# Kernel optimization log

Measured on AMD Instinct MI355X. Metric: run time of the kernel, lower is better.

The kernel has to match this reference:

```python
import jax, jax.numpy as jnp
import numpy as np
from jax import lax

B = 256
C1 = 256          # conv1 channels
NUM_CAPS = 32     # primary capsule types
CAP_DIM = 8       # primary capsule dim
NUM_PRIMARY = NUM_CAPS * 6 * 6  # 1152
NUM_OUT = 10
OUT_DIM = 16
NUM_ROUTING = 3


def squash(v):
    # v: (..., d)
    sq = jnp.sum(v * v, axis=-1, keepdims=True)
    scale = sq / (1.0 + sq)
    return scale * v / jnp.sqrt(sq + 1e-8)


def setup_inputs() -> dict:
    key = jax.random.key(0)
    k = jax.random.split(key, 6)
    x = jax.random.normal(k[0], (B, 1, 28, 28), dtype=jnp.float32)
    # kaiming fan_out init for convs
    conv1_w = jax.random.normal(k[1], (C1, 1, 9, 9), dtype=jnp.float32) * np.sqrt(2.0 / (C1 * 81))
    conv1_b = jnp.zeros((C1,), dtype=jnp.float32)
    pc_out = NUM_CAPS * CAP_DIM  # 256
    pc_w = jax.random.normal(k[2], (pc_out, C1, 9, 9), dtype=jnp.float32) * np.sqrt(2.0 / (pc_out * 81))
    pc_b = jnp.zeros((pc_out,), dtype=jnp.float32)
    W_digit = jax.random.normal(k[3], (NUM_PRIMARY, CAP_DIM, NUM_OUT, OUT_DIM), dtype=jnp.float32) * 0.01
    return {"x": x, "conv1_w": conv1_w, "conv1_b": conv1_b,
            "pc_w": pc_w, "pc_b": pc_b, "W_digit": W_digit}


def _conv(x, w, b, stride):
    y = lax.conv_general_dilated(x, w, (stride, stride), 'VALID',
                                 dimension_numbers=('NCHW', 'OIHW', 'NCHW'))
    return y + b[None, :, None, None]


def reference(x, conv1_w, conv1_b, pc_w, pc_b, W_digit):
    # conv1 + ReLU: (B,1,28,28) -> (B,256,20,20)
    h = jax.nn.relu(_conv(x, conv1_w, conv1_b, 1))
    # primary caps conv: -> (B, 256, 6, 6)
    p = _conv(h, pc_w, pc_b, 2)
    bsz, _, oh, ow = p.shape
    # (B, num_caps, cap_dim, H, W) -> (B, num_caps, H, W, cap_dim) -> (B, N, d)
    p = p.reshape(bsz, NUM_CAPS, CAP_DIM, oh, ow)
    p = jnp.transpose(p, (0, 1, 3, 4, 2)).reshape(bsz, NUM_CAPS * oh * ow, CAP_DIM)
    u = squash(p)  # (B, 1152, 8)
    # dynamic routing
    u_hat = jnp.einsum('bid,idjo->bijo', u, W_digit)  # (B, 1152, 10, 16)
    b_logits = jnp.zeros((bsz, NUM_PRIMARY, NUM_OUT, 1), dtype=u_hat.dtype)
    v = None
    for it in range(NUM_ROUTING):
        c = jax.nn.softmax(b_logits, axis=2)
        s = jnp.sum(c * u_hat, axis=1)          # (B, 10, 16)
        v = squash(s)
        if it < NUM_ROUTING - 1:
            agreement = jnp.sum(u_hat * v[:, None, :, :], axis=-1, keepdims=True)
            b_logits = b_logits + agreement
    return v
```

## Files before the change

kernel.cpp:

```cpp
#include <hip/hip_runtime.h>
#include <hip/hip_bf16.h>

#define NI 1152

typedef __attribute__((ext_vector_type(8))) _Float16 f16x8;
typedef __attribute__((ext_vector_type(4))) float f32x4;
typedef __attribute__((ext_vector_type(8))) unsigned short u16x8;
typedef __attribute__((ext_vector_type(4))) unsigned short u16x4;

static const size_t UHAT_OFF = 0;
static const size_t W5_OFF   = 0;
static const size_t H3_OFF   = 10747904UL;
static const size_t WT1_OFF  = 63176704UL;
static const size_t PP_OFF   = 63259648UL;
static const size_t U_OFF    = 94371840UL;
static const size_t SP_OFF   = 103809024UL;
static const size_t L_OFF    = 127401984UL;
static const size_t V_OFF    = 139198464UL;

__device__ __forceinline__ unsigned short f2bf(float x) {
    unsigned u = __builtin_bit_cast(unsigned, x);
    u += 0x7fffu + ((u >> 16) & 1u);
    return (unsigned short)(u >> 16);
}
__device__ __forceinline__ float bf2f(unsigned short h) {
    return __builtin_bit_cast(float, (unsigned)h << 16);
}
__device__ __forceinline__ void atomAddF(float* p, float v) {
    __hip_atomic_fetch_add(p, v, __ATOMIC_RELAXED, __HIP_MEMORY_SCOPE_AGENT);
}

#define GLD16(gsrc, ldst)                                                      \
    __builtin_amdgcn_global_load_lds(                                          \
        (__attribute__((address_space(1))) const void*)(gsrc),                 \
        (__attribute__((address_space(3))) void*)(ldst), 16, 0, 0)

__global__ __launch_bounds__(256) void k_prep_w(const float* __restrict__ pcw,
                                                _Float16* __restrict__ w5) {
    __shared__ float sl[5184];
    int oc  = blockIdx.x;
    int ic0 = blockIdx.y * 64;
    const float* src = pcw + (size_t)oc * 20736 + (size_t)ic0 * 81;
    for (int j = threadIdx.x; j < 5184; j += 256) sl[j] = src[j];
    __syncthreads();
    int nt = oc >> 7, row = oc & 127;
    for (int t = threadIdx.x; t < 5184; t += 256) {
        int tap = t >> 6, i = t & 63;
        int ic = ic0 + i;
        int ks = ic >> 5, p = (ic >> 3) & 3, icl = ic & 7;
        w5[((size_t)(((tap * 8 + ks) * 2 + nt) * 4 + p) * 128 + row) * 8 + icl] =
            (_Float16)sl[i * 81 + tap];
    }
}

__global__ void k_transpose_w1(const float* __restrict__ w, float* __restrict__ wT) {
    int t = blockIdx.x, oc = threadIdx.x;
    wT[t * 256 + oc] = w[oc * 81 + t];
}

__global__ __launch_bounds__(256) void k_conv1(const float* __restrict__ x,
                                               const float* __restrict__ wT1,
                                               const float* __restrict__ bias,
                                               _Float16* __restrict__ h3) {
    __shared__ _Float16 hs[2][20][256];
    int b  = blockIdx.y;
    int rp = blockIdx.x;
    int oc = threadIdx.x;
    int oy0 = rp * 2;
    const float* xb = x + (size_t)b * 784;
    float bv = bias[oc];
    float acc0[20], acc1[20];
#pragma unroll
    for (int i = 0; i < 20; ++i) { acc0[i] = bv; acc1[i] = bv; }
    for (int ky = 0; ky < 9; ++ky) {
        const float* r0 = xb + (oy0 + ky) * 28;
        const float* r1 = r0 + 28;
        float x0[28], x1[28];
#pragma unroll
        for (int c = 0; c < 28; ++c) { x0[c] = r0[c]; x1[c] = r1[c]; }
#pragma unroll
        for (int kx = 0; kx < 9; ++kx) {
            float w = wT1[(ky * 9 + kx) * 256 + oc];
#pragma unroll
            for (int px = 0; px < 20; ++px) {
                acc0[px] += x0[px + kx] * w;
                acc1[px] += x1[px + kx] * w;
            }
        }
    }
#pragma unroll
    for (int px = 0; px < 20; ++px) {
        hs[0][px][oc] = (_Float16)fmaxf(acc0[px], 0.f);
        hs[1][px][oc] = (_Float16)fmaxf(acc1[px], 0.f);
    }
    __syncthreads();
    for (int cid = threadIdx.x; cid < 1280; cid += 256) {
        int kp = cid & 31;
        int pos = cid >> 5;
        int ry = pos / 20, px2 = pos % 20;
        int ks = kp >> 2, p = kp & 3;
        f16x8 val = *(const f16x8*)&hs[ry][px2][ks * 32 + p * 8];
        _Float16* dst = h3 + ((size_t)((ks * 400 + (oy0 + ry) * 20 + px2) * 4 + p) * 256 + b) * 8;
        *(f16x8*)dst = val;
    }
}

__global__ __launch_bounds__(256, 4) void k_conv2_mfma(
    const _Float16* __restrict__ h3, const _Float16* __restrict__ w5,
    float* __restrict__ pp) {
    __shared__ _Float16 As[8192], Bs[8192];
    const int mt = blockIdx.x, nt = blockIdx.y, ks = blockIdx.z;
    const int pos = mt >> 1, bhalf = mt & 1;
    const int py = pos / 6, px = pos % 6;
    const int l = threadIdx.x & 63;
    const int w = __builtin_amdgcn_readfirstlane((int)(threadIdx.x >> 6));
    const int wm = w >> 1, wn = w & 1;

    f32x4 acc[4][4];
    const f32x4 z = {0.f, 0.f, 0.f, 0.f};
#pragma unroll
    for (int mi = 0; mi < 4; ++mi)
#pragma unroll
        for (int ni = 0; ni < 4; ++ni) acc[mi][ni] = z;

    const int ch = (l >> 4) * 1024;
    const int am = (wm * 64 + (l & 15)) * 8;
    const int bn = (wn * 64 + (l & 15)) * 8;
    const int lds_off = w * 1024 + l * 8;

    for (int it = 0; it < 41; ++it) {
        const int t0 = 2 * it, t1 = t0 + 1;
        const int tA1 = (t1 > 80) ? 80 : t1;
#pragma unroll
        for (int tl = 0; tl < 2; ++tl) {
            const int tap  = tl ? t1 : t0;
            const int tapA = tl ? tA1 : t0;
            const int y = 2 * py + tapA / 9, xx = 2 * px + tapA % 9;
            const _Float16* asrc = h3 + ((size_t)(ks * 400 + y * 20 + xx) * 4 + w) * 2048 +
                                   bhalf * 1024 + l * 8;
            const _Float16* bsrc = w5 + ((size_t)((tap * 8 + ks) * 2 + nt)) * 4096 + lds_off;
            GLD16(asrc,       As + tl * 4096 + lds_off);
            GLD16(asrc + 512, As + tl * 4096 + lds_off + 512);
            GLD16(bsrc,       Bs + tl * 4096 + lds_off);
            GLD16(bsrc + 512, Bs + tl * 4096 + lds_off + 512);
        }
        __syncthreads();
#pragma unroll
        for (int s = 0; s < 2; ++s) {
            const int pb = s * 4096 + ch;
            f16x8 a[4], b[4];
#pragma unroll
            for (int i = 0; i < 4; ++i) {
                a[i] = *(const f16x8*)(As + pb + am + i * 128);
                b[i] = *(const f16x8*)(Bs + pb + bn + i * 128);
            }
#pragma unroll
            for (int mi = 0; mi < 4; ++mi)
#pragma unroll
                for (int ni = 0; ni < 4; ++ni)
                    acc[mi][ni] = __builtin_amdgcn_mfma_f32_16x16x32_f16(a[mi], b[ni], acc[mi][ni], 0, 0, 0);
        }
        __syncthreads();
    }
    const int row0 = (l >> 4) * 4;
    const int ncol = l & 15;
#pragma unroll
    for (int mi = 0; mi < 4; ++mi)
#pragma unroll
        for (int ni = 0; ni < 4; ++ni) {
            int n = nt * 128 + wn * 64 + ni * 16 + ncol;
#pragma unroll
            for (int reg = 0; reg < 4; ++reg) {
                int m = pos * 256 + bhalf * 128 + wm * 64 + mi * 16 + row0 + reg;
                atomAddF(&pp[(size_t)m * 256 + n], acc[mi][ni][reg]);
            }
        }
}

__global__ __launch_bounds__(256) void k_sum_squash2(const float* __restrict__ pp,
                                                     const float* __restrict__ bias,
                                                     float* __restrict__ u) {
    int m = blockIdx.x * 8 + (threadIdx.x >> 5);
    int cap = threadIdx.x & 31;
    const float* p0 = pp + (size_t)m * 256 + cap * 8;
    float s[8], sq = 0.f;
#pragma unroll
    for (int d = 0; d < 8; ++d) {
        float a = p0[d] + bias[cap * 8 + d];
        sq += a * a; s[d] = a;
    }
    float scale = sq / ((1.0f + sq) * sqrtf(sq + 1e-8f));
    int pos = m >> 8, b = m & 255;
    int i = cap * 36 + pos;
    float* up = u + ((size_t)i * 256 + b) * 8;
    ((float4*)up)[0] = make_float4(scale * s[0], scale * s[1], scale * s[2], scale * s[3]);
    ((float4*)up)[1] = make_float4(scale * s[4], scale * s[5], scale * s[6], scale * s[7]);
}

__global__ __launch_bounds__(256) void k_build_uhat(const float* __restrict__ u,
                                                    const float* __restrict__ W,
                                                    unsigned short* __restrict__ UH) {
    __shared__ float Ws[1280];
    int i = blockIdx.x;
    for (int t = threadIdx.x; t < 1280; t += 256) Ws[t] = W[(size_t)i * 1280 + t];
    __syncthreads();
    int b = threadIdx.x;
    const float* uptr = u + ((size_t)i * 256 + b) * 8;
    float u8[8];
    ((float4*)u8)[0] = ((const float4*)uptr)[0];
    ((float4*)u8)[1] = ((const float4*)uptr)[1];
#pragma unroll
    for (int j = 0; j < 10; ++j) {
        float o16[16];
#pragma unroll
        for (int o = 0; o < 16; ++o) o16[o] = 0.f;
#pragma unroll
        for (int d = 0; d < 8; ++d) {
            const float* wp = Ws + d * 160 + j * 16;
#pragma unroll
            for (int o = 0; o < 16; ++o) o16[o] += u8[d] * wp[o];
        }
        u16x8 h0, h1;
#pragma unroll
        for (int o = 0; o < 8; ++o) { h0[o] = f2bf(o16[o]); h1[o] = f2bf(o16[8 + o]); }
        unsigned short* dst = UH + ((size_t)(i * 10 + j) * 256 + b) * 16;
        *(u16x8*)dst = h0;
        *(u16x8*)(dst + 8) = h1;
    }
}

__global__ __launch_bounds__(256) void k_route_s0(const unsigned short* __restrict__ UH,
                                                  float* __restrict__ SP) {
    int it = blockIdx.x, bt = blockIdx.y;
    int b0 = bt * 64, i0 = it * 8;
    int b_l = threadIdx.x & 63;
    int og = __builtin_amdgcn_readfirstlane((int)(threadIdx.x >> 6));
    float acc[10][4];
#pragma unroll
    for (int j = 0; j < 10; ++j)
#pragma unroll
        for (int o = 0; o < 4; ++o) acc[j][o] = 0.f;
    for (int li = 0; li < 8; ++li) {
        const unsigned short* up = UH + ((size_t)(i0 + li) * 10 * 256 + b0 + b_l) * 16 + og * 4;
#pragma unroll
        for (int j = 0; j < 10; ++j) {
            u16x4 t = *(const u16x4*)(up + j * 4096);
#pragma unroll
            for (int o = 0; o < 4; ++o) acc[j][o] += bf2f(t[o]);
        }
    }
    float* sp = SP + ((size_t)it * 256 + b0 + b_l) * 160 + og * 4;
#pragma unroll
    for (int j = 0; j < 10; ++j)
        *(float4*)(sp + j * 16) = make_float4(0.1f * acc[j][0], 0.1f * acc[j][1],
                                              0.1f * acc[j][2], 0.1f * acc[j][3]);
}

__global__ __launch_bounds__(256) void k_route_s(const float* __restrict__ L,
                                                 const unsigned short* __restrict__ UH,
                                                 float* __restrict__ SP) {
    __shared__ float LG[64][81];
    int it = blockIdx.x, bt = blockIdx.y;
    int b0 = bt * 64, i0 = it * 8;
    int b_l = threadIdx.x & 63;
    int og = __builtin_amdgcn_readfirstlane((int)(threadIdx.x >> 6));
    int b_r = threadIdx.x >> 2, part = threadIdx.x & 3;
    {
        const float4* lsrc = (const float4*)(L + (size_t)(b0 + b_r) * 11520 + i0 * 10 + part * 20);
#pragma unroll
        for (int q = 0; q < 5; ++q) {
            float4 t = lsrc[q]; int c = part * 20 + q * 4;
            LG[b_r][c] = t.x; LG[b_r][c + 1] = t.y; LG[b_r][c + 2] = t.z; LG[b_r][c + 3] = t.w;
        }
    }
    __syncthreads();
    float acc[10][4];
#pragma unroll
    for (int j = 0; j < 10; ++j)
#pragma unroll
        for (int o = 0; o < 4; ++o) acc[j][o] = 0.f;
    for (int li = 0; li < 8; ++li) {
        float lg[10];
#pragma unroll
        for (int j = 0; j < 10; ++j) lg[j] = LG[b_l][li * 10 + j];
        float m = lg[0];
#pragma unroll
        for (int j = 1; j < 10; ++j) m = fmaxf(m, lg[j]);
        float e[10], ssum = 0.f;
#pragma unroll
        for (int j = 0; j < 10; ++j) { e[j] = __expf(lg[j] - m); ssum += e[j]; }
        float inv = 1.0f / ssum;
        const unsigned short* up = UH + ((size_t)(i0 + li) * 10 * 256 + b0 + b_l) * 16 + og * 4;
#pragma unroll
        for (int j = 0; j < 10; ++j) {
            float cj = e[j] * inv;
            u16x4 t = *(const u16x4*)(up + j * 4096);
#pragma unroll
            for (int o = 0; o < 4; ++o) acc[j][o] += cj * bf2f(t[o]);
        }
    }
    float* sp = SP + ((size_t)it * 256 + b0 + b_l) * 160 + og * 4;
#pragma unroll
    for (int j = 0; j < 10; ++j)
        *(float4*)(sp + j * 16) = make_float4(acc[j][0], acc[j][1], acc[j][2], acc[j][3]);
}

__global__ __launch_bounds__(256) void k_route_v(const float* __restrict__ SP,
                                                 float* __restrict__ vout) {
    int n = blockIdx.x * 256 + threadIdx.x;
    float ssum = 0.f;
    for (int t = 0; t < 144; ++t) ssum += SP[(size_t)t * 40960 + n];
    float sq = ssum * ssum;
    float tot = sq;
#pragma unroll
    for (int mask = 1; mask < 16; mask <<= 1) tot += __shfl_xor(tot, mask, 64);
    float scale = tot / ((1.0f + tot) * sqrtf(tot + 1e-8f));
    vout[n] = scale * ssum;
}

__global__ __launch_bounds__(256) void k_route_agree(float* __restrict__ L,
                                                     const unsigned short* __restrict__ UH,
                                                     const float* __restrict__ V,
                                                     int add) {
    __shared__ float VL[64][165];
    __shared__ float LG[64][81];
    int it = blockIdx.x, bt = blockIdx.y;
    int b0 = bt * 64, i0 = it * 8;
    int b_l = threadIdx.x & 63;
    int ig = __builtin_amdgcn_readfirstlane((int)(threadIdx.x >> 6));
    int b_r = threadIdx.x >> 2, part = threadIdx.x & 3;
    {
        const float4* vsrc = (const float4*)(V + (size_t)(b0 + b_r) * 160 + part * 40);
#pragma unroll
        for (int q = 0; q < 10; ++q) {
            float4 vv = vsrc[q]; int c = part * 40 + q * 4;
            VL[b_r][c] = vv.x; VL[b_r][c + 1] = vv.y; VL[b_r][c + 2] = vv.z; VL[b_r][c + 3] = vv.w;
        }
        if (add) {
            const float4* lsrc = (const float4*)(L + (size_t)(b0 + b_r) * 11520 + i0 * 10 + part * 20);
#pragma unroll
            for (int q = 0; q < 5; ++q) {
                float4 t = lsrc[q]; int c = part * 20 + q * 4;
                LG[b_r][c] = t.x; LG[b_r][c + 1] = t.y; LG[b_r][c + 2] = t.z; LG[b_r][c + 3] = t.w;
            }
        }
    }
    __syncthreads();
#pragma unroll
    for (int ii = 0; ii < 2; ++ii) {
        int il = ig * 2 + ii;
        int i = i0 + il;
        const unsigned short* up = UH + ((size_t)i * 10 * 256 + b0 + b_l) * 16;
#pragma unroll
        for (int j = 0; j < 10; ++j) {
            u16x8 ua = *(const u16x8*)(up + j * 4096);
            u16x8 ub = *(const u16x8*)(up + j * 4096 + 8);
            float a = 0.f;
#pragma unroll
            for (int o = 0; o < 8; ++o) a += bf2f(ua[o]) * VL[b_l][j * 16 + o];
#pragma unroll
            for (int o = 0; o < 8; ++o) a += bf2f(ub[o]) * VL[b_l][j * 16 + 8 + o];
            float base = add ? LG[b_l][il * 10 + j] : 0.f;
            LG[b_l][il * 10 + j] = base + a;
        }
    }
    __syncthreads();
    {
        float4* ldst = (float4*)(L + (size_t)(b0 + b_r) * 11520 + i0 * 10 + part * 20);
#pragma unroll
        for (int q = 0; q < 5; ++q) {
            int c = part * 20 + q * 4;
            ldst[q] = make_float4(LG[b_r][c], LG[b_r][c + 1], LG[b_r][c + 2], LG[b_r][c + 3]);
        }
    }
}

extern "C" void kernel_launch(void* const* d_in, const int* in_sizes, int n_in,
                              void* d_out, int out_size, void* d_ws, size_t ws_size,
                              hipStream_t stream) {
    (void)in_sizes; (void)n_in; (void)out_size; (void)ws_size;
    const float* x   = (const float*)d_in[0];
    const float* c1w = (const float*)d_in[1];
    const float* c1b = (const float*)d_in[2];
    const float* pcw = (const float*)d_in[3];
    const float* pcb = (const float*)d_in[4];
    const float* Wd  = (const float*)d_in[5];
    float* out = (float*)d_out;
    char* wsb  = (char*)d_ws;

    unsigned short* uh = (unsigned short*)(wsb + UHAT_OFF);
    _Float16* w5 = (_Float16*)(wsb + W5_OFF);
    _Float16* h3 = (_Float16*)(wsb + H3_OFF);
    float* wT1 = (float*)(wsb + WT1_OFF);
    float* pp  = (float*)(wsb + PP_OFF);
    float* u   = (float*)(wsb + U_OFF);
    float* sp  = (float*)(wsb + SP_OFF);
    float* lg  = (float*)(wsb + L_OFF);
    float* v   = (float*)(wsb + V_OFF);

    hipMemsetAsync(pp, 0, (size_t)9216 * 256 * sizeof(float), stream);
    hipMemsetAsync(w5 + (size_t)81 * 65536, 0, (size_t)65536 * sizeof(_Float16), stream);

    k_prep_w<<<dim3(256, 4), 256, 0, stream>>>(pcw, w5);
    k_transpose_w1<<<81, 256, 0, stream>>>(c1w, wT1);
    k_conv1<<<dim3(10, 256), 256, 0, stream>>>(x, wT1, c1b, h3);
    k_conv2_mfma<<<dim3(72, 2, 8), 256, 0, stream>>>(h3, w5, pp);
    k_sum_squash2<<<1152, 256, 0, stream>>>(pp, pcb, u);
    k_build_uhat<<<1152, 256, 0, stream>>>(u, Wd, uh);

    k_route_s0<<<dim3(144, 4), 256, 0, stream>>>(uh, sp);
    k_route_v<<<160, 256, 0, stream>>>(sp, v);
    k_route_agree<<<dim3(144, 4), 256, 0, stream>>>(lg, uh, v, 0);
    k_route_s<<<dim3(144, 4), 256, 0, stream>>>(lg, uh, sp);
    k_route_v<<<160, 256, 0, stream>>>(sp, v);
    k_route_agree<<<dim3(144, 4), 256, 0, stream>>>(lg, uh, v, 1);
    k_route_s<<<dim3(144, 4), 256, 0, stream>>>(lg, uh, sp);
    k_route_v<<<160, 256, 0, stream>>>(sp, out);
}
```

Baseline: 474.7 us.

## Load conv2 MFMA operands directly to registers and fuse routing agree with softmax-sum

The primary-capsule conv now reads A and B fragments straight from global memory into registers with a three-stage software pipeline. This replaces the LDS staging and barriers, and the weights are re-laid out so each lane's fragment is contiguous. The routing agreement and the next iteration's softmax-weighted sum are fused into one kernel that reuses the logits held in LDS, which removes a kernel launch and a global round trip of the logits per iteration. The trade-off is heavier register pressure (occupancy hint lowered to 2) and less global-load coalescing and reuse for the A operand.

```diff
diff --git a/kernel.cpp b/kernel.cpp
--- a/kernel.cpp
+++ b/kernel.cpp
@@ -9,7 +9,7 @@
 typedef __attribute__((ext_vector_type(4))) unsigned short u16x4;
 
 static const size_t UHAT_OFF = 0;
-static const size_t W5_OFF   = 0;
+static const size_t W6_OFF   = 0;
 static const size_t H3_OFF   = 10747904UL;
 static const size_t WT1_OFF  = 63176704UL;
 static const size_t PP_OFF   = 63259648UL;
@@ -30,25 +30,21 @@
     __hip_atomic_fetch_add(p, v, __ATOMIC_RELAXED, __HIP_MEMORY_SCOPE_AGENT);
 }
 
-#define GLD16(gsrc, ldst)                                                      \
-    __builtin_amdgcn_global_load_lds(                                          \
-        (__attribute__((address_space(1))) const void*)(gsrc),                 \
-        (__attribute__((address_space(3))) void*)(ldst), 16, 0, 0)
-
 __global__ __launch_bounds__(256) void k_prep_w(const float* __restrict__ pcw,
-                                                _Float16* __restrict__ w5) {
+                                                _Float16* __restrict__ w6) {
     __shared__ float sl[5184];
     int oc  = blockIdx.x;
     int ic0 = blockIdx.y * 64;
     const float* src = pcw + (size_t)oc * 20736 + (size_t)ic0 * 81;
     for (int j = threadIdx.x; j < 5184; j += 256) sl[j] = src[j];
     __syncthreads();
-    int nt = oc >> 7, row = oc & 127;
+    int og = oc >> 4, fr = oc & 15;
     for (int t = threadIdx.x; t < 5184; t += 256) {
         int tap = t >> 6, i = t & 63;
         int ic = ic0 + i;
-        int ks = ic >> 5, p = (ic >> 3) & 3, icl = ic & 7;
-        w5[((size_t)(((tap * 8 + ks) * 2 + nt) * 4 + p) * 128 + row) * 8 + icl] =
+        int ks = ic >> 5, kch = (ic >> 3) & 3, icl = ic & 7;
+        int lane = kch * 16 + fr;
+        w6[(((size_t)(tap * 8 + ks) * 16 + og) * 64 + lane) * 8 + icl] =
             (_Float16)sl[i * 81 + tap];
     }
 }
@@ -105,17 +101,22 @@
     }
 }
 
-__global__ __launch_bounds__(256, 4) void k_conv2_mfma(
-    const _Float16* __restrict__ h3, const _Float16* __restrict__ w5,
+__global__ __launch_bounds__(256, 2) void k_conv2_direct(
+    const _Float16* __restrict__ h3, const _Float16* __restrict__ w6,
     float* __restrict__ pp) {
-    __shared__ _Float16 As[8192], Bs[8192];
     const int mt = blockIdx.x, nt = blockIdx.y, ks = blockIdx.z;
     const int pos = mt >> 1, bhalf = mt & 1;
     const int py = pos / 6, px = pos % 6;
     const int l = threadIdx.x & 63;
-    const int w = __builtin_amdgcn_readfirstlane((int)(threadIdx.x >> 6));
+    const int w = threadIdx.x >> 6;
     const int wm = w >> 1, wn = w & 1;
-
+    const int p = l >> 4, fr = l & 15;
+
+    const _Float16* abase = h3 + (size_t)ks * 3276800 + p * 2048 +
+                            (bhalf * 128 + wm * 64 + fr) * 8;
+    const _Float16* bbase = w6 + (nt * 8 + wn * 4) * 512 + l * 8;
+
+    f16x8 a[3][4], b[3][4];
     f32x4 acc[4][4];
     const f32x4 z = {0.f, 0.f, 0.f, 0.f};
 #pragma unroll
@@ -123,45 +124,44 @@
 #pragma unroll
         for (int ni = 0; ni < 4; ++ni) acc[mi][ni] = z;
 
-    const int ch = (l >> 4) * 1024;
-    const int am = (wm * 64 + (l & 15)) * 8;
-    const int bn = (wn * 64 + (l & 15)) * 8;
-    const int lds_off = w * 1024 + l * 8;
-
-    for (int it = 0; it < 41; ++it) {
-        const int t0 = 2 * it, t1 = t0 + 1;
-        const int tA1 = (t1 > 80) ? 80 : t1;
-#pragma unroll
-        for (int tl = 0; tl < 2; ++tl) {
-            const int tap  = tl ? t1 : t0;
-            const int tapA = tl ? tA1 : t0;
-            const int y = 2 * py + tapA / 9, xx = 2 * px + tapA % 9;
-            const _Float16* asrc = h3 + ((size_t)(ks * 400 + y * 20 + xx) * 4 + w) * 2048 +
-                                   bhalf * 1024 + l * 8;
-            const _Float16* bsrc = w5 + ((size_t)((tap * 8 + ks) * 2 + nt)) * 4096 + lds_off;
-            GLD16(asrc,       As + tl * 4096 + lds_off);
-            GLD16(asrc + 512, As + tl * 4096 + lds_off + 512);
-            GLD16(bsrc,       Bs + tl * 4096 + lds_off);
-            GLD16(bsrc + 512, Bs + tl * 4096 + lds_off + 512);
-        }
-        __syncthreads();
-#pragma unroll
-        for (int s = 0; s < 2; ++s) {
-            const int pb = s * 4096 + ch;
-            f16x8 a[4], b[4];
-#pragma unroll
-            for (int i = 0; i < 4; ++i) {
-                a[i] = *(const f16x8*)(As + pb + am + i * 128);
-                b[i] = *(const f16x8*)(Bs + pb + bn + i * 128);
-            }
-#pragma unroll
-            for (int mi = 0; mi < 4; ++mi)
-#pragma unroll
-                for (int ni = 0; ni < 4; ++ni)
-                    acc[mi][ni] = __builtin_amdgcn_mfma_f32_16x16x32_f16(a[mi], b[ni], acc[mi][ni], 0, 0, 0);
-        }
-        __syncthreads();
-    }
+#define LOADAB(buf, tap)                                                       \
+    do {                                                                       \
+        const int _t = (tap);                                                  \
+        const int _y = _t / 9, _x = _t - _y * 9;                               \
+        const _Float16* _ab = abase + ((2 * py + _y) * 20 + (2 * px + _x)) * 8192; \
+        a[buf][0] = *(const f16x8*)(_ab);                                      \
+        a[buf][1] = *(const f16x8*)(_ab + 128);                                \
+        a[buf][2] = *(const f16x8*)(_ab + 256);                                \
+        a[buf][3] = *(const f16x8*)(_ab + 384);                                \
+        const _Float16* _bb = bbase + (size_t)(_t * 8 + ks) * 8192;            \
+        b[buf][0] = *(const f16x8*)(_bb);                                      \
+        b[buf][1] = *(const f16x8*)(_bb + 512);                                \
+        b[buf][2] = *(const f16x8*)(_bb + 1024);                               \
+        b[buf][3] = *(const f16x8*)(_bb + 1536);                               \
+    } while (0)
+
+#define MFMA_ALL(buf)                                                          \
+    do {                                                                       \
+        _Pragma("unroll") for (int mi = 0; mi < 4; ++mi)                       \
+            _Pragma("unroll") for (int ni = 0; ni < 4; ++ni)                   \
+                acc[mi][ni] = __builtin_amdgcn_mfma_f32_16x16x32_f16(          \
+                    a[buf][mi], b[buf][ni], acc[mi][ni], 0, 0, 0);             \
+    } while (0)
+
+    LOADAB(0, 0);
+    LOADAB(1, 1);
+    for (int k = 0; k < 27; ++k) {
+        const int t0 = 3 * k;
+        LOADAB(2, t0 + 2);
+        MFMA_ALL(0);
+        if (t0 + 3 < 81) LOADAB(0, t0 + 3);
+        MFMA_ALL(1);
+        if (t0 + 4 < 81) LOADAB(1, t0 + 4);
+        MFMA_ALL(2);
+    }
+#undef LOADAB
+#undef MFMA_ALL
+
     const int row0 = (l >> 4) * 4;
     const int ncol = l & 15;
 #pragma unroll
@@ -256,72 +256,11 @@
                                               0.1f * acc[j][2], 0.1f * acc[j][3]);
 }
 
-__global__ __launch_bounds__(256) void k_route_s(const float* __restrict__ L,
-                                                 const unsigned short* __restrict__ UH,
-                                                 float* __restrict__ SP) {
-    __shared__ float LG[64][81];
-    int it = blockIdx.x, bt = blockIdx.y;
-    int b0 = bt * 64, i0 = it * 8;
-    int b_l = threadIdx.x & 63;
-    int og = __builtin_amdgcn_readfirstlane((int)(threadIdx.x >> 6));
-    int b_r = threadIdx.x >> 2, part = threadIdx.x & 3;
-    {
-        const float4* lsrc = (const float4*)(L + (size_t)(b0 + b_r) * 11520 + i0 * 10 + part * 20);
-#pragma unroll
-        for (int q = 0; q < 5; ++q) {
-            float4 t = lsrc[q]; int c = part * 20 + q * 4;
-            LG[b_r][c] = t.x; LG[b_r][c + 1] = t.y; LG[b_r][c + 2] = t.z; LG[b_r][c + 3] = t.w;
-        }
-    }
-    __syncthreads();
-    float acc[10][4];
-#pragma unroll
-    for (int j = 0; j < 10; ++j)
-#pragma unroll
-        for (int o = 0; o < 4; ++o) acc[j][o] = 0.f;
-    for (int li = 0; li < 8; ++li) {
-        float lg[10];
-#pragma unroll
-        for (int j = 0; j < 10; ++j) lg[j] = LG[b_l][li * 10 + j];
-        float m = lg[0];
-#pragma unroll
-        for (int j = 1; j < 10; ++j) m = fmaxf(m, lg[j]);
-        float e[10], ssum = 0.f;
-#pragma unroll
-        for (int j = 0; j < 10; ++j) { e[j] = __expf(lg[j] - m); ssum += e[j]; }
-        float inv = 1.0f / ssum;
-        const unsigned short* up = UH + ((size_t)(i0 + li) * 10 * 256 + b0 + b_l) * 16 + og * 4;
-#pragma unroll
-        for (int j = 0; j < 10; ++j) {
-            float cj = e[j] * inv;
-            u16x4 t = *(const u16x4*)(up + j * 4096);
-#pragma unroll
-            for (int o = 0; o < 4; ++o) acc[j][o] += cj * bf2f(t[o]);
-        }
-    }
-    float* sp = SP + ((size_t)it * 256 + b0 + b_l) * 160 + og * 4;
-#pragma unroll
-    for (int j = 0; j < 10; ++j)
-        *(float4*)(sp + j * 16) = make_float4(acc[j][0], acc[j][1], acc[j][2], acc[j][3]);
-}
-
-__global__ __launch_bounds__(256) void k_route_v(const float* __restrict__ SP,
-                                                 float* __restrict__ vout) {
-    int n = blockIdx.x * 256 + threadIdx.x;
-    float ssum = 0.f;
-    for (int t = 0; t < 144; ++t) ssum += SP[(size_t)t * 40960 + n];
-    float sq = ssum * ssum;
-    float tot = sq;
-#pragma unroll
-    for (int mask = 1; mask < 16; mask <<= 1) tot += __shfl_xor(tot, mask, 64);
-    float scale = tot / ((1.0f + tot) * sqrtf(tot + 1e-8f));
-    vout[n] = scale * ssum;
-}
-
-__global__ __launch_bounds__(256) void k_route_agree(float* __restrict__ L,
-                                                     const unsigned short* __restrict__ UH,
-                                                     const float* __restrict__ V,
-                                                     int add) {
+__global__ __launch_bounds__(256) void k_route_as(float* __restrict__ L,
+                                                  const unsigned short* __restrict__ UH,
+                                                  const float* __restrict__ V,
+                                                  float* __restrict__ SP,
+                                                  int add, int storeL) {
     __shared__ float VL[64][165];
     __shared__ float LG[64][81];
     int it = blockIdx.x, bt = blockIdx.y;
@@ -365,7 +304,7 @@
         }
     }
     __syncthreads();
-    {
+    if (storeL) {
         float4* ldst = (float4*)(L + (size_t)(b0 + b_r) * 11520 + i0 * 10 + part * 20);
 #pragma unroll
         for (int q = 0; q < 5; ++q) {
@@ -373,6 +312,48 @@
             ldst[q] = make_float4(LG[b_r][c], LG[b_r][c + 1], LG[b_r][c + 2], LG[b_r][c + 3]);
         }
     }
+    float acc[10][4];
+#pragma unroll
+    for (int j = 0; j < 10; ++j)
+#pragma unroll
+        for (int o = 0; o < 4; ++o) acc[j][o] = 0.f;
+    for (int li = 0; li < 8; ++li) {
+        float lg[10];
+#pragma unroll
+        for (int j = 0; j < 10; ++j) lg[j] = LG[b_l][li * 10 + j];
+        float m = lg[0];
+#pragma unroll
+        for (int j = 1; j < 10; ++j) m = fmaxf(m, lg[j]);
+        float e[10], ssum = 0.f;
+#pragma unroll
+        for (int j = 0; j < 10; ++j) { e[j] = __expf(lg[j] - m); ssum += e[j]; }
+        float inv = 1.0f / ssum;
+        const unsigned short* up = UH + ((size_t)(i0 + li) * 10 * 256 + b0 + b_l) * 16 + ig * 4;
+#pragma unroll
+        for (int j = 0; j < 10; ++j) {
+            float cj = e[j] * inv;
+            u16x4 t = *(const u16x4*)(up + j * 4096);
+#pragma unroll
+            for (int o = 0; o < 4; ++o) acc[j][o] += cj * bf2f(t[o]);
+        }
+    }
+    float* sp = SP + ((size_t)it * 256 + b0 + b_l) * 160 + ig * 4;
+#pragma unroll
+    for (int j = 0; j < 10; ++j)
+        *(float4*)(sp + j * 16) = make_float4(acc[j][0], acc[j][1], acc[j][2], acc[j][3]);
+}
+
+__global__ __launch_bounds__(256) void k_route_v(const float* __restrict__ SP,
+                                                 float* __restrict__ vout) {
+    int n = blockIdx.x * 256 + threadIdx.x;
+    float ssum = 0.f;
+    for (int t = 0; t < 144; ++t) ssum += SP[(size_t)t * 40960 + n];
+    float sq = ssum * ssum;
+    float tot = sq;
+#pragma unroll
+    for (int mask = 1; mask < 16; mask <<= 1) tot += __shfl_xor(tot, mask, 64);
+    float scale = tot / ((1.0f + tot) * sqrtf(tot + 1e-8f));
+    vout[n] = scale * ssum;
 }
 
 extern "C" void kernel_launch(void* const* d_in, const int* in_sizes, int n_in,
@@ -389,7 +370,7 @@
     char* wsb  = (char*)d_ws;
 
     unsigned short* uh = (unsigned short*)(wsb + UHAT_OFF);
-    _Float16* w5 = (_Float16*)(wsb + W5_OFF);
+    _Float16* w6 = (_Float16*)(wsb + W6_OFF);
     _Float16* h3 = (_Float16*)(wsb + H3_OFF);
     float* wT1 = (float*)(wsb + WT1_OFF);
     float* pp  = (float*)(wsb + PP_OFF);
@@ -399,21 +380,18 @@
     float* v   = (float*)(wsb + V_OFF);
 
     hipMemsetAsync(pp, 0, (size_t)9216 * 256 * sizeof(float), stream);
-    hipMemsetAsync(w5 + (size_t)81 * 65536, 0, (size_t)65536 * sizeof(_Float16), stream);
-
-    k_prep_w<<<dim3(256, 4), 256, 0, stream>>>(pcw, w5);
+
+    k_prep_w<<<dim3(256, 4), 256, 0, stream>>>(pcw, w6);
     k_transpose_w1<<<81, 256, 0, stream>>>(c1w, wT1);
     k_conv1<<<dim3(10, 256), 256, 0, stream>>>(x, wT1, c1b, h3);
-    k_conv2_mfma<<<dim3(72, 2, 8), 256, 0, stream>>>(h3, w5, pp);
+    k_conv2_direct<<<dim3(72, 2, 8), 256, 0, stream>>>(h3, w6, pp);
     k_sum_squash2<<<1152, 256, 0, stream>>>(pp, pcb, u);
     k_build_uhat<<<1152, 256, 0, stream>>>(u, Wd, uh);
 
     k_route_s0<<<dim3(144, 4), 256, 0, stream>>>(uh, sp);
     k_route_v<<<160, 256, 0, stream>>>(sp, v);
-    k_route_agree<<<dim3(144, 4), 256, 0, stream>>>(lg, uh, v, 0);
-    k_route_s<<<dim3(144, 4), 256, 0, stream>>>(lg, uh, sp);
+    k_route_as<<<dim3(144, 4), 256, 0, stream>>>(lg, uh, v, sp, 0, 1);
     k_route_v<<<160, 256, 0, stream>>>(sp, v);
-    k_route_agree<<<dim3(144, 4), 256, 0, stream>>>(lg, uh, v, 1);
-    k_route_s<<<dim3(144, 4), 256, 0, stream>>>(lg, uh, sp);
+    k_route_as<<<dim3(144, 4), 256, 0, stream>>>(lg, uh, v, sp, 1, 0);
     k_route_v<<<160, 256, 0, stream>>>(sp, out);
 }
```

New measurement: 461.9 us. -2.7%, faster.
